# Kernel optimization log

Hardware: AMD Instinct MI355X
Metric: run time of the kernel (lower is better)

## Reference

```python
import jax, jax.numpy as jnp
import numpy as np

B, T, E, H, L = 16, 1024, 1024, 512, 6
C = 1024  # conv out channels


def _lstm_dir(x_tbi, Wih, Whh, bih, bhh):
    # x_tbi: [T, B, I]; single-direction LSTM, PyTorch gate order (i, f, g, o)
    Bn = x_tbi.shape[1]
    Hh = Whh.shape[1]
    b = bih + bhh
    def step(carry, xt):
        h, c = carry
        g = xt @ Wih.T + h @ Whh.T + b  # [B, 4H]
        i, f, gg, o = jnp.split(g, 4, axis=-1)
        c = jax.nn.sigmoid(f) * c + jax.nn.sigmoid(i) * jnp.tanh(gg)
        h = jax.nn.sigmoid(o) * jnp.tanh(c)
        return (h, c), h
    h0 = jnp.zeros((Bn, Hh), x_tbi.dtype)
    _, hs = jax.lax.scan(step, (h0, h0), x_tbi)
    return hs  # [T, B, H]


def _forward(embeddings, attention_mask, labels, conv_w, conv_b, bn_gamma, bn_beta,
             bn_mean, bn_var, lstm_Wih, lstm_Whh, lstm_bih, lstm_bhh,
             cls_w, cls_b, crf_start, crf_end, crf_trans):
    # Conv1d(E->1024, k=5, pad=2) on [B, C, T]
    x = jax.lax.conv_general_dilated(
        embeddings.astype(jnp.float32).transpose(0, 2, 1), conv_w,
        window_strides=(1,), padding=[(2, 2)],
        dimension_numbers=("NCH", "OIH", "NCH")) + conv_b[None, :, None]
    # BatchNorm1d (eval: running stats) fused + ReLU
    scale = bn_gamma / jnp.sqrt(bn_var + 1e-5)
    x = jax.nn.relu(x * scale[None, :, None] + (bn_beta - bn_mean * scale)[None, :, None])
    # time-major for the LSTM scans: [T, B, 1024]
    x = x.transpose(2, 0, 1)
    for l in range(3):
        fw = _lstm_dir(x, lstm_Wih[l, 0], lstm_Whh[l, 0], lstm_bih[l, 0], lstm_bhh[l, 0])
        bw = _lstm_dir(x[::-1], lstm_Wih[l, 1], lstm_Whh[l, 1], lstm_bih[l, 1], lstm_bhh[l, 1])[::-1]
        x = jnp.concatenate([fw, bw], axis=-1)  # [T, B, 2H]
    logits = x @ cls_w.T + cls_b  # [T, B, L]; dropout is identity in eval
    # CRF negative log-likelihood (torchcrf, batch_first handled by time-major layout)
    mask = (attention_mask.astype(bool) & (labels != -100)).T  # [T, B]
    tags = jnp.where(labels == -100, 0, labels).astype(jnp.int32).T  # [T, B]
    mf = mask.astype(logits.dtype)
    bidx = jnp.arange(logits.shape[1])
    # numerator: score of the given tag sequence
    score0 = crf_start[tags[0]] + logits[0, bidx, tags[0]]
    def num_step(carry, inp):
        score, prev = carry
        et, mt, mtf, tt = inp
        s = crf_trans[prev, tt] + et[bidx, tt]
        return (score + mtf * s, jnp.where(mt, tt, prev)), None
    (num, last), _ = jax.lax.scan(
        num_step, (score0, tags[0]), (logits[1:], mask[1:], mf[1:], tags[1:]))
    num = num + crf_end[last]
    # denominator: forward algorithm (log partition)
    def den_step(alpha, inp):
        et, mt = inp
        nxt = jax.nn.logsumexp(alpha[:, :, None] + crf_trans[None, :, :] + et[:, None, :], axis=1)
        return jnp.where(mt[:, None], nxt, alpha), None
    alpha, _ = jax.lax.scan(den_step, crf_start + logits[0], (logits[1:], mask[1:]))
    den = jax.nn.logsumexp(alpha + crf_end, axis=-1)
    return -(num - den).mean()  # reduction='mean' over batch, negated


def setup_inputs() -> dict:
    key = jax.random.key(0)
    ks = jax.random.split(key, 16)
    p = lambda k, shp: jax.random.normal(k, shp, jnp.float32) * 0.05
    return {
        "embeddings": jax.random.normal(ks[0], (B, T, E), jnp.float32),
        "attention_mask": jnp.ones((B, T), jnp.int32),
        "labels": jax.random.randint(ks[1], (B, T), 0, L, jnp.int32),
        "conv_w": p(ks[2], (C, E, 5)),
        "conv_b": p(ks[3], (C,)),
        "bn_gamma": jnp.ones((C,), jnp.float32),
        "bn_beta": jnp.zeros((C,), jnp.float32),
        "bn_mean": p(ks[4], (C,)),
        "bn_var": jax.random.uniform(ks[5], (C,), jnp.float32, 0.5, 1.5),
        "lstm_Wih": p(ks[6], (3, 2, 4 * H, C)),
        "lstm_Whh": p(ks[7], (3, 2, 4 * H, H)),
        "lstm_bih": p(ks[8], (3, 2, 4 * H)),
        "lstm_bhh": p(ks[9], (3, 2, 4 * H)),
        "cls_w": p(ks[10], (L, 2 * H)),
        "cls_b": p(ks[11], (L,)),
        "crf_start": p(ks[12], (L,)),
        "crf_end": p(ks[13], (L,)),
        "crf_trans": p(ks[14], (L, L)),
    }


def reference(embeddings, attention_mask, labels, conv_w, conv_b, bn_gamma, bn_beta,
              bn_mean, bn_var, lstm_Wih, lstm_Whh, lstm_bih, lstm_bhh,
              cls_w, cls_b, crf_start, crf_end, crf_trans):
    return _forward(embeddings, attention_mask, labels, conv_w, conv_b, bn_gamma,
                    bn_beta, bn_mean, bn_var, lstm_Wih, lstm_Whh, lstm_bih,
                    lstm_bhh, cls_w, cls_b, crf_start, crf_end, crf_trans)
```

## Files before the change

kernel.cpp:

```cpp
#include <hip/hip_runtime.h>


typedef short bf16_t;
typedef __attribute__((ext_vector_type(8))) short bf16x8;
typedef __attribute__((ext_vector_type(4))) float f32x4;

__device__ __forceinline__ bf16_t f2b(float x) {
  unsigned u = __float_as_uint(x);
  unsigned r = (u + 0x7fffu + ((u >> 16) & 1u)) >> 16;
  return (bf16_t)(unsigned short)r;
}
__device__ __forceinline__ float blo(unsigned u) { return __uint_as_float(u << 16); }
__device__ __forceinline__ float bhi(unsigned u) { return __uint_as_float(u & 0xffff0000u); }


__global__ void embed_pad_k(const float* __restrict__ E, bf16_t* __restrict__ P) {
  size_t i4 = ((size_t)blockIdx.x * 256 + threadIdx.x) * 4;
  if (i4 >= 16ul * 1028 * 1024) return;
  int e = (int)(i4 & 1023);
  size_t rest = i4 >> 10;
  int tp = (int)(rest % 1028);
  int b  = (int)(rest / 1028);
  bf16_t o[4];
  if (tp >= 2 && tp < 1026) {
    const float4 v = *(const float4*)(E + (((size_t)b * 1024 + (tp - 2)) * 1024 + e));
    o[0] = f2b(v.x); o[1] = f2b(v.y); o[2] = f2b(v.z); o[3] = f2b(v.w);
  } else {
    o[0] = o[1] = o[2] = o[3] = 0;
  }
  *(uint2*)(P + i4) = *(const uint2*)o;
}

__global__ void convw_cvt_k(const float* __restrict__ S, bf16_t* __restrict__ D) {
  int idx = blockIdx.x * 256 + threadIdx.x;
  if (idx >= 1024 * 1024) return;
  int c = idx >> 10, e = idx & 1023;
  const float* s = S + (size_t)idx * 5;
#pragma unroll
  for (int kk = 0; kk < 5; kk++) D[(size_t)c * 5120 + kk * 1024 + e] = f2b(s[kk]);
}

__global__ void bnfold_k(const float* cb, const float* g, const float* be,
                         const float* mn, const float* vr, float* a, float* dd) {
  int c = blockIdx.x * 256 + threadIdx.x;
  if (c < 1024) {
    float s = g[c] * rsqrtf(vr[c] + 1e-5f);
    a[c] = s;
    dd[c] = (cb[c] - mn[c]) * s + be[c];
  }
}

__global__ void wihcvt_k(const float* __restrict__ S, bf16_t* __restrict__ D) {
  size_t i = ((size_t)blockIdx.x * 256 + threadIdx.x) * 4;
  if (i >= 3ul * 2 * 2048 * 1024) return;
  float4 v = *(const float4*)(S + i);
  bf16_t o[4] = {f2b(v.x), f2b(v.y), f2b(v.z), f2b(v.w)};
  *(uint2*)(D + i) = *(const uint2*)o;
}

__global__ __launch_bounds__(256, 1) void gemm_bt(
    const bf16_t* __restrict__ A, const bf16_t* __restrict__ W,
    const float* __restrict__ bias0, const float* __restrict__ bias1,
    bf16_t* __restrict__ C, int M, int N, int K) {
  const int tid = threadIdx.x;
  const int nb = N >> 7;
  const int m0 = (blockIdx.x / nb) * 128, n0 = (blockIdx.x % nb) * 128;
  __shared__ bf16_t As[128][72];
  __shared__ bf16_t Bs[128][72];
  const int wv = tid >> 6, ln = tid & 63;
  const int wm = (wv >> 1) * 64, wn = (wv & 1) * 64;
  const int lb = ln & 15, lq = ln >> 4;
  f32x4 acc[4][4] = {};
  for (int k0 = 0; k0 < K; k0 += 64) {
    __syncthreads();
#pragma unroll
    for (int i = 0; i < 4; i++) {
      int idx = tid + i * 256, r = idx >> 3, ch = idx & 7;
      *(uint4*)&As[r][ch * 8] = *(const uint4*)(A + (size_t)(m0 + r) * K + k0 + ch * 8);
      *(uint4*)&Bs[r][ch * 8] = *(const uint4*)(W + (size_t)(n0 + r) * K + k0 + ch * 8);
    }
    __syncthreads();
#pragma unroll
    for (int kk = 0; kk < 2; kk++) {
      bf16x8 af[4], bfr[4];
#pragma unroll
      for (int t = 0; t < 4; t++) {
        af[t]  = *(const bf16x8*)&As[wm + t * 16 + lb][kk * 32 + lq * 8];
        bfr[t] = *(const bf16x8*)&Bs[wn + t * 16 + lb][kk * 32 + lq * 8];
      }
#pragma unroll
      for (int mt = 0; mt < 4; mt++)
#pragma unroll
        for (int nt = 0; nt < 4; nt++)
          acc[mt][nt] = __builtin_amdgcn_mfma_f32_16x16x32_bf16(af[mt], bfr[nt], acc[mt][nt], 0, 0, 0);
    }
  }
#pragma unroll
  for (int mt = 0; mt < 4; mt++)
#pragma unroll
    for (int nt = 0; nt < 4; nt++) {
      int col = n0 + wn + nt * 16 + lb;
      float bs = bias0[col] + bias1[col];
#pragma unroll
      for (int r = 0; r < 4; r++) {
        int row = m0 + wm + mt * 16 + lq * 4 + r;
        C[(size_t)row * N + col] = f2b(acc[mt][nt][r] + bs);
      }
    }
}

__global__ __launch_bounds__(256, 1) void conv_gemm(
    const bf16_t* __restrict__ EP, const bf16_t* __restrict__ Wc,
    const float* __restrict__ bn_a, const float* __restrict__ bn_d,
    bf16_t* __restrict__ X) {
  const int tid = threadIdx.x;
  const int m0 = (blockIdx.x >> 3) * 128, n0 = (blockIdx.x & 7) * 128;
  __shared__ bf16_t As[128][72];
  __shared__ bf16_t Bs[128][72];
  const int wv = tid >> 6, ln = tid & 63;
  const int wm = (wv >> 1) * 64, wn = (wv & 1) * 64;
  const int lb = ln & 15, lq = ln >> 4;
  f32x4 acc[4][4] = {};
  for (int kk = 0; kk < 5; kk++) {
    for (int k0 = 0; k0 < 1024; k0 += 64) {
      __syncthreads();
#pragma unroll
      for (int i = 0; i < 4; i++) {
        int idx = tid + i * 256, r = idx >> 3, ch = idx & 7;
        int m = m0 + r;
        const bf16_t* ap = EP + ((size_t)((m & 15) * 1028 + (m >> 4) + kk)) * 1024 + k0 + ch * 8;
        *(uint4*)&As[r][ch * 8] = *(const uint4*)ap;
        *(uint4*)&Bs[r][ch * 8] = *(const uint4*)(Wc + (size_t)(n0 + r) * 5120 + kk * 1024 + k0 + ch * 8);
      }
      __syncthreads();
#pragma unroll
      for (int kq = 0; kq < 2; kq++) {
        bf16x8 af[4], bfr[4];
#pragma unroll
        for (int t = 0; t < 4; t++) {
          af[t]  = *(const bf16x8*)&As[wm + t * 16 + lb][kq * 32 + lq * 8];
          bfr[t] = *(const bf16x8*)&Bs[wn + t * 16 + lb][kq * 32 + lq * 8];
        }
#pragma unroll
        for (int mt = 0; mt < 4; mt++)
#pragma unroll
          for (int nt = 0; nt < 4; nt++)
            acc[mt][nt] = __builtin_amdgcn_mfma_f32_16x16x32_bf16(af[mt], bfr[nt], acc[mt][nt], 0, 0, 0);
      }
    }
  }
#pragma unroll
  for (int mt = 0; mt < 4; mt++)
#pragma unroll
    for (int nt = 0; nt < 4; nt++) {
      int col = n0 + wn + nt * 16 + lb;
      float sa = bn_a[col], sd = bn_d[col];
#pragma unroll
      for (int r = 0; r < 4; r++) {
        int row = m0 + wm + mt * 16 + lq * 4 + r;
        float v = fmaxf(acc[mt][nt][r] * sa + sd, 0.f);
        X[(size_t)row * 1024 + col] = f2b(v);
      }
    }
}

__global__ __launch_bounds__(256, 1) void rec_kernel(
    const float* __restrict__ Whh,
    const bf16_t* __restrict__ gfw,
    const bf16_t* __restrict__ gbw,
    bf16_t* __restrict__ xout,
    unsigned long long* __restrict__ hstT,
    float* __restrict__ cst,
    int t0f, int t0b, int nsteps, int tag_base) {
  const int tid = threadIdx.x;
  const int d  = blockIdx.x >> 5;
  const int j0 = (blockIdx.x & 31) << 4;
  const int wv = tid >> 6;
  const int ln = tid & 63;
  const int lb = ln & 15;
  const int lq = ln >> 4;

  __shared__ bf16_t Hb[16][520];
  __shared__ float  Ex[4][16][17];

  bf16x8 afrag[16];
  {
    const float* wrow = Whh + ((size_t)(d * 2048 + wv * 512 + j0 + lb)) * 512;
#pragma unroll
    for (int kk = 0; kk < 16; kk++) {
      const float* wp = wrow + kk * 32 + lq * 8;
      float4 va = *(const float4*)wp;
      float4 vb = *(const float4*)(wp + 4);
      bf16x8 fr;
      fr[0] = f2b(va.x); fr[1] = f2b(va.y); fr[2] = f2b(va.z); fr[3] = f2b(va.w);
      fr[4] = f2b(vb.x); fr[5] = f2b(vb.y); fr[6] = f2b(vb.z); fr[7] = f2b(vb.w);
      afrag[kk] = fr;
    }
  }
  const int cb = tid >> 4;
  const int cj = tid & 15;
  float creg = cst[((size_t)d * 16 + cb) * 512 + j0 + cj];
  const bf16_t* gates = (d == 0) ? gfw : gbw;

  unsigned g0, g1;
  {
    const int trow = (d == 0) ? 0 : (nsteps - 1);
    const unsigned* gp = (const unsigned*)(gates + ((size_t)trow * 16 + lb) * 2048 + wv * 512 + j0 + lq * 4);
    g0 = gp[0]; g1 = gp[1];
  }

  for (int s = 0; s < nsteps; s++) {
    const int rb = (s & 1) ^ 1, wb = s & 1;
    {
      const unsigned long long* src =
          hstT + (((size_t)rb * 2 + d) * 16 + (wv << 2)) * 256;
      const unsigned expect = (unsigned)(tag_base + s);
      unsigned long long v[16];
      bool ok;
      do {
        ok = true;
#pragma unroll
        for (int i = 0; i < 16; i++)
          v[i] = __hip_atomic_load(src + i * 64 + ln, __ATOMIC_RELAXED, __HIP_MEMORY_SCOPE_AGENT);
#pragma unroll
        for (int i = 0; i < 16; i++) ok = ok && ((unsigned)(v[i] >> 32) == expect);
      } while (!__all(ok));
#pragma unroll
      for (int i = 0; i < 16; i++) {
        int idx = i * 64 + ln;
        *(unsigned*)&Hb[(wv << 2) + (idx >> 8)][(idx & 255) * 2] = (unsigned)v[i];
      }
    }
    __syncthreads();
    const int t = (d == 0) ? (t0f + s) : (t0b + nsteps - 1 - s);
    f32x4 acc0, acc1;
    acc0[0] = blo(g0); acc0[1] = bhi(g0); acc0[2] = blo(g1); acc0[3] = bhi(g1);
    acc1[0] = 0.f; acc1[1] = 0.f; acc1[2] = 0.f; acc1[3] = 0.f;
#pragma unroll
    for (int kk = 0; kk < 8; kk++) {
      bf16x8 b0 = *(const bf16x8*)&Hb[lb][(2 * kk) * 32 + lq * 8];
      bf16x8 b1 = *(const bf16x8*)&Hb[lb][(2 * kk + 1) * 32 + lq * 8];
      acc0 = __builtin_amdgcn_mfma_f32_16x16x32_bf16(afrag[2 * kk], b0, acc0, 0, 0, 0);
      acc1 = __builtin_amdgcn_mfma_f32_16x16x32_bf16(afrag[2 * kk + 1], b1, acc1, 0, 0, 0);
    }
    if (s + 1 < nsteps) {
      const int trn = (d == 0) ? (s + 1) : (nsteps - 2 - s);
      const unsigned* gpn = (const unsigned*)(gates + ((size_t)trn * 16 + lb) * 2048 + wv * 512 + j0 + lq * 4);
      g0 = gpn[0]; g1 = gpn[1];
    }
#pragma unroll
    for (int r = 0; r < 4; r++) Ex[wv][lq * 4 + r][lb] = acc0[r] + acc1[r];
    __syncthreads();
    float gi = Ex[0][cj][cb], gf = Ex[1][cj][cb], gg = Ex[2][cj][cb], go = Ex[3][cj][cb];
    float si = 1.f / (1.f + expf(-gi));
    float sf = 1.f / (1.f + expf(-gf));
    float so = 1.f / (1.f + expf(-go));
    creg = sf * creg + si * tanhf(gg);
    float h = so * tanhf(creg);
    bf16_t hb = f2b(h);
    {
      int hi = __shfl_down((int)(unsigned)(unsigned short)hb, 1, 64);
      if ((cj & 1) == 0) {
        unsigned data = (unsigned)(unsigned short)hb | ((unsigned)hi << 16);
        unsigned long long val =
            ((unsigned long long)(unsigned)(tag_base + s + 1) << 32) | data;
        unsigned long long* hp =
            hstT + (((size_t)wb * 2 + d) * 16 + cb) * 256 + ((j0 + cj) >> 1);
        __hip_atomic_store(hp, val, __ATOMIC_RELAXED, __HIP_MEMORY_SCOPE_AGENT);
      }
    }
    xout[((size_t)t * 16 + cb) * 1024 + d * 512 + j0 + cj] = hb;
  }
  cst[((size_t)d * 16 + cb) * 512 + j0 + cj] = creg;
}

__global__ void cls_kernel(const bf16_t* __restrict__ X, const float* __restrict__ Wc,
                           const float* __restrict__ bc, float* __restrict__ Lg) {
  int wv = threadIdx.x >> 6, ln = threadIdx.x & 63;
  size_t m = (size_t)blockIdx.x * 4 + wv;
  const bf16_t* xr = X + m * 1024 + ln * 16;
  uint4 v0 = *(const uint4*)xr;
  uint4 v1 = *(const uint4*)(xr + 8);
  float xv[16];
  const unsigned* p0 = (const unsigned*)&v0;
  const unsigned* p1 = (const unsigned*)&v1;
#pragma unroll
  for (int i = 0; i < 4; i++) { xv[2 * i] = blo(p0[i]); xv[2 * i + 1] = bhi(p0[i]); }
#pragma unroll
  for (int i = 0; i < 4; i++) { xv[8 + 2 * i] = blo(p1[i]); xv[8 + 2 * i + 1] = bhi(p1[i]); }
#pragma unroll
  for (int l = 0; l < 6; l++) {
    const float* wr = Wc + l * 1024 + ln * 16;
    float p = 0.f;
#pragma unroll
    for (int i = 0; i < 16; i++) p += xv[i] * wr[i];
#pragma unroll
    for (int off = 32; off; off >>= 1) p += __shfl_xor(p, off, 64);
    if (ln == 0) Lg[m * 6 + l] = p + bc[l];
  }
}

__global__ void crf_kernel(const float* __restrict__ Lg, const int* __restrict__ attn,
                           const int* __restrict__ labels, const float* __restrict__ start,
                           const float* __restrict__ endw, const float* __restrict__ trans,
                           float* __restrict__ out) {
  int b = blockIdx.x, ln = threadIdx.x;
  __shared__ float str[36];
  __shared__ int tg[1024];
  __shared__ unsigned char mk[1024];
  if (ln < 36) str[ln] = trans[ln];
  for (int t = ln; t < 1024; t += 64) {
    int lab = labels[b * 1024 + t];
    mk[t] = (unsigned char)((attn[b * 1024 + t] != 0) && (lab != -100));
    tg[t] = (lab == -100) ? 0 : lab;
  }
  __syncthreads();
  int j = ln;
  bool act = j < 6;
  float alpha = act ? (start[j] + Lg[(size_t)b * 6 + j]) : -1e30f;
  for (int t = 1; t < 1024; t++) {
    float vv[6], mx = -1e30f;
#pragma unroll
    for (int i = 0; i < 6; i++) {
      float ai = __shfl(alpha, i, 64);
      float v = ai + str[i * 6 + (act ? j : 0)];
      vv[i] = v;
      mx = fmaxf(mx, v);
    }
    float sm = 0.f;
#pragma unroll
    for (int i = 0; i < 6; i++) sm += expf(vv[i] - mx);
    float na = mx + logf(sm) + (act ? Lg[((size_t)t * 16 + b) * 6 + j] : 0.f);
    if (mk[t] && act) alpha = na;
  }
  float z = act ? (alpha + endw[j]) : -1e30f;
  float zm = z;
#pragma unroll
  for (int i = 0; i < 6; i++) zm = fmaxf(zm, __shfl(z, i, 64));
  float zs = act ? expf(z - zm) : 0.f;
  float tot = 0.f;
#pragma unroll
  for (int i = 0; i < 6; i++) tot += __shfl(zs, i, 64);
  float den = zm + logf(tot);
  if (ln == 0) {
    float score = start[tg[0]] + Lg[(size_t)b * 6 + tg[0]];
    int prev = tg[0];
    for (int t = 1; t < 1024; t++) {
      if (mk[t]) {
        score += str[prev * 6 + tg[t]] + Lg[((size_t)t * 16 + b) * 6 + tg[t]];
        prev = tg[t];
      }
    }
    score += endw[prev];
    atomicAdd(out, (den - score) * (1.0f / 16.0f));
  }
}

extern "C" void kernel_launch(void* const* d_in, const int* in_sizes, int n_in,
                              void* d_out, int out_size, void* d_ws, size_t ws_size,
                              hipStream_t stream) {
  const float* emb    = (const float*)d_in[0];
  const int*   attn   = (const int*)d_in[1];
  const int*   labels = (const int*)d_in[2];
  const float* convw  = (const float*)d_in[3];
  const float* convb  = (const float*)d_in[4];
  const float* bng    = (const float*)d_in[5];
  const float* bnb    = (const float*)d_in[6];
  const float* bnm    = (const float*)d_in[7];
  const float* bnv    = (const float*)d_in[8];
  const float* wih    = (const float*)d_in[9];
  const float* whh    = (const float*)d_in[10];
  const float* bih    = (const float*)d_in[11];
  const float* bhh    = (const float*)d_in[12];
  const float* clsw   = (const float*)d_in[13];
  const float* clsb   = (const float*)d_in[14];
  const float* crfs   = (const float*)d_in[15];
  const float* crfe   = (const float*)d_in[16];
  const float* crft   = (const float*)d_in[17];
  (void)in_sizes; (void)n_in; (void)out_size; (void)ws_size;

  char* w = (char*)d_ws;
  auto alloc = [&](size_t bytes) { char* p = w; w += (bytes + 255) & ~(size_t)255; return p; };
  bf16_t* emb_pad = (bf16_t*)alloc(16ul * 1028 * 1024 * 2);
  bf16_t* wconv   = (bf16_t*)alloc(1024ul * 5120 * 2);
  float*  bn_a    = (float*)alloc(4096);
  float*  bn_d    = (float*)alloc(4096);
  bf16_t* wihb    = (bf16_t*)alloc(3ul * 2 * 2048 * 1024 * 2);
  bf16_t* xA      = (bf16_t*)alloc(16384ul * 1024 * 2);
  bf16_t* xB      = (bf16_t*)alloc(16384ul * 1024 * 2);
  bf16_t* gfw     = (bf16_t*)alloc(8192ul * 2048 * 2);
  bf16_t* gbw     = (bf16_t*)alloc(8192ul * 2048 * 2);
  unsigned long long* hstT = (unsigned long long*)alloc(2ul * 2 * 16 * 256 * 8);
  float*  cst     = (float*)alloc(2ul * 16 * 512 * 4);
  float*  lgt     = (float*)alloc(16384ul * 6 * 4);

  hipMemsetAsync(d_out, 0, 4, stream);

  embed_pad_k<<<16448, 256, 0, stream>>>(emb, emb_pad);
  convw_cvt_k<<<4096, 256, 0, stream>>>(convw, wconv);
  bnfold_k<<<4, 256, 0, stream>>>(convb, bng, bnb, bnm, bnv, bn_a, bn_d);
  wihcvt_k<<<12288, 256, 0, stream>>>(wih, wihb);

  conv_gemm<<<128 * 8, 256, 0, stream>>>(emb_pad, wconv, bn_a, bn_d, xA);

  bf16_t* xin = xA;
  bf16_t* xout = xB;
  for (int l = 0; l < 3; l++) {
    hipMemsetAsync(hstT, 0, 2ul * 2 * 16 * 256 * 8, stream);
    hipMemsetAsync(cst, 0, 2ul * 16 * 512 * 4, stream);
    for (int c = 0; c < 2; c++) {
      int t0f = c * 512, t0b = (1 - c) * 512;
      gemm_bt<<<64 * 16, 256, 0, stream>>>(
          xin + (size_t)t0f * 16 * 1024, wihb + ((size_t)l * 2 + 0) * 2048 * 1024,
          bih + (l * 2 + 0) * 2048, bhh + (l * 2 + 0) * 2048, gfw, 8192, 2048, 1024);
      gemm_bt<<<64 * 16, 256, 0, stream>>>(
          xin + (size_t)t0b * 16 * 1024, wihb + ((size_t)l * 2 + 1) * 2048 * 1024,
          bih + (l * 2 + 1) * 2048, bhh + (l * 2 + 1) * 2048, gbw, 8192, 2048, 1024);
      rec_kernel<<<64, 256, 0, stream>>>(whh + (size_t)l * 2 * 2048 * 512,
                                         gfw, gbw, xout, hstT, cst, t0f, t0b, 512, c * 512);
    }
    bf16_t* tmp = xin; xin = xout; xout = tmp;
  }

  cls_kernel<<<4096, 256, 0, stream>>>(xin, clsw, clsb, lgt);
  crf_kernel<<<16, 64, 0, stream>>>(lgt, attn, labels, crfs, crfe, crft, (float*)d_out);
}
```

Baseline: 9.208 ms.

## Interleave LSTM gate rows so each lane holds i,f,g,o and drop LDS exchange

The W_hh rows loaded into each wave's MFMA fragments are permuted so that the four gate outputs of one hidden unit land in the same lane's accumulator. This removes the per-step LDS exchange buffer and the second __syncthreads in the recurrent loop. The input-gate GEMM epilogue now writes gates in a [t][j][b][gate] layout so each lane fetches its four gate preactivations with one 8-byte load. The spin-wait also re-polls only the entries whose tags are stale. The cost is scattered 2-byte stores in the GEMM epilogue and a changed hidden-state packing via a shuffle across lanes 16 apart.

After: 11.84 ms. 1.29x slower.

```diff
diff --git a/kernel.cpp b/kernel.cpp
--- a/kernel.cpp
+++ b/kernel.cpp
@@ -58,26 +58,25 @@
   *(uint2*)(D + i) = *(const uint2*)o;
 }
 
-__global__ __launch_bounds__(256, 1) void gemm_bt(
+__global__ __launch_bounds__(256, 1) void gemm_gates(
     const bf16_t* __restrict__ A, const bf16_t* __restrict__ W,
     const float* __restrict__ bias0, const float* __restrict__ bias1,
-    bf16_t* __restrict__ C, int M, int N, int K) {
+    bf16_t* __restrict__ G) {
   const int tid = threadIdx.x;
-  const int nb = N >> 7;
-  const int m0 = (blockIdx.x / nb) * 128, n0 = (blockIdx.x % nb) * 128;
+  const int m0 = (blockIdx.x >> 4) * 128, n0 = (blockIdx.x & 15) * 128;
   __shared__ bf16_t As[128][72];
   __shared__ bf16_t Bs[128][72];
   const int wv = tid >> 6, ln = tid & 63;
   const int wm = (wv >> 1) * 64, wn = (wv & 1) * 64;
   const int lb = ln & 15, lq = ln >> 4;
   f32x4 acc[4][4] = {};
-  for (int k0 = 0; k0 < K; k0 += 64) {
+  for (int k0 = 0; k0 < 1024; k0 += 64) {
     __syncthreads();
 #pragma unroll
     for (int i = 0; i < 4; i++) {
       int idx = tid + i * 256, r = idx >> 3, ch = idx & 7;
-      *(uint4*)&As[r][ch * 8] = *(const uint4*)(A + (size_t)(m0 + r) * K + k0 + ch * 8);
-      *(uint4*)&Bs[r][ch * 8] = *(const uint4*)(W + (size_t)(n0 + r) * K + k0 + ch * 8);
+      *(uint4*)&As[r][ch * 8] = *(const uint4*)(A + (size_t)(m0 + r) * 1024 + k0 + ch * 8);
+      *(uint4*)&Bs[r][ch * 8] = *(const uint4*)(W + (size_t)(n0 + r) * 1024 + k0 + ch * 8);
     }
     __syncthreads();
 #pragma unroll
@@ -100,11 +99,13 @@
 #pragma unroll
     for (int nt = 0; nt < 4; nt++) {
       int col = n0 + wn + nt * 16 + lb;
+      int g = col >> 9, j = col & 511;
       float bs = bias0[col] + bias1[col];
 #pragma unroll
       for (int r = 0; r < 4; r++) {
         int row = m0 + wm + mt * 16 + lq * 4 + r;
-        C[(size_t)row * N + col] = f2b(acc[mt][nt][r] + bs);
+        int t = row >> 4, b = row & 15;
+        G[(((size_t)t * 512 + j) * 16 + b) * 4 + g] = f2b(acc[mt][nt][r] + bs);
       }
     }
 }
@@ -166,8 +167,8 @@
 
 __global__ __launch_bounds__(256, 1) void rec_kernel(
     const float* __restrict__ Whh,
-    const bf16_t* __restrict__ gfw,
-    const bf16_t* __restrict__ gbw,
+    const bf16_t* __restrict__ Gfw,
+    const bf16_t* __restrict__ Gbw,
     bf16_t* __restrict__ xout,
     unsigned long long* __restrict__ hstT,
     float* __restrict__ cst,
@@ -180,12 +181,12 @@
   const int lb = ln & 15;
   const int lq = ln >> 4;
 
-  __shared__ bf16_t Hb[16][520];
-  __shared__ float  Ex[4][16][17];
+  __shared__ bf16_t Hb[16][514];
 
   bf16x8 afrag[16];
   {
-    const float* wrow = Whh + ((size_t)(d * 2048 + wv * 512 + j0 + lb)) * 512;
+    const float* wrow =
+        Whh + ((size_t)(d * 2048 + (lb & 3) * 512 + j0 + wv * 4 + (lb >> 2))) * 512;
 #pragma unroll
     for (int kk = 0; kk < 16; kk++) {
       const float* wp = wrow + kk * 32 + lq * 8;
@@ -197,16 +198,14 @@
       afrag[kk] = fr;
     }
   }
-  const int cb = tid >> 4;
-  const int cj = tid & 15;
-  float creg = cst[((size_t)d * 16 + cb) * 512 + j0 + cj];
-  const bf16_t* gates = (d == 0) ? gfw : gbw;
-
-  unsigned g0, g1;
+  const int jme = j0 + wv * 4 + lq;
+  float creg = cst[((size_t)d * 16 + lb) * 512 + jme];
+  const bf16_t* G = (d == 0) ? Gfw : Gbw;
+
+  uint2 gv;
   {
     const int trow = (d == 0) ? 0 : (nsteps - 1);
-    const unsigned* gp = (const unsigned*)(gates + ((size_t)trow * 16 + lb) * 2048 + wv * 512 + j0 + lq * 4);
-    g0 = gp[0]; g1 = gp[1];
+    gv = *(const uint2*)(G + (((size_t)trow * 512 + jme) * 16 + lb) * 4);
   }
 
   for (int s = 0; s < nsteps; s++) {
@@ -216,15 +215,19 @@
           hstT + (((size_t)rb * 2 + d) * 16 + (wv << 2)) * 256;
       const unsigned expect = (unsigned)(tag_base + s);
       unsigned long long v[16];
-      bool ok;
-      do {
-        ok = true;
+#pragma unroll
+      for (int i = 0; i < 16; i++)
+        v[i] = __hip_atomic_load(src + i * 64 + ln, __ATOMIC_RELAXED, __HIP_MEMORY_SCOPE_AGENT);
+      while (true) {
+        bool ok = true;
+#pragma unroll
+        for (int i = 0; i < 16; i++) ok = ok && ((unsigned)(v[i] >> 32) == expect);
+        if (__all(ok)) break;
 #pragma unroll
         for (int i = 0; i < 16; i++)
-          v[i] = __hip_atomic_load(src + i * 64 + ln, __ATOMIC_RELAXED, __HIP_MEMORY_SCOPE_AGENT);
-#pragma unroll
-        for (int i = 0; i < 16; i++) ok = ok && ((unsigned)(v[i] >> 32) == expect);
-      } while (!__all(ok));
+          if ((unsigned)(v[i] >> 32) != expect)
+            v[i] = __hip_atomic_load(src + i * 64 + ln, __ATOMIC_RELAXED, __HIP_MEMORY_SCOPE_AGENT);
+      }
 #pragma unroll
       for (int i = 0; i < 16; i++) {
         int idx = i * 64 + ln;
@@ -234,7 +237,7 @@
     __syncthreads();
     const int t = (d == 0) ? (t0f + s) : (t0b + nsteps - 1 - s);
     f32x4 acc0, acc1;
-    acc0[0] = blo(g0); acc0[1] = bhi(g0); acc0[2] = blo(g1); acc0[3] = bhi(g1);
+    acc0[0] = blo(gv.x); acc0[1] = bhi(gv.x); acc0[2] = blo(gv.y); acc0[3] = bhi(gv.y);
     acc1[0] = 0.f; acc1[1] = 0.f; acc1[2] = 0.f; acc1[3] = 0.f;
 #pragma unroll
     for (int kk = 0; kk < 8; kk++) {
@@ -245,13 +248,10 @@
     }
     if (s + 1 < nsteps) {
       const int trn = (d == 0) ? (s + 1) : (nsteps - 2 - s);
-      const unsigned* gpn = (const unsigned*)(gates + ((size_t)trn * 16 + lb) * 2048 + wv * 512 + j0 + lq * 4);
-      g0 = gpn[0]; g1 = gpn[1];
-    }
-#pragma unroll
-    for (int r = 0; r < 4; r++) Ex[wv][lq * 4 + r][lb] = acc0[r] + acc1[r];
-    __syncthreads();
-    float gi = Ex[0][cj][cb], gf = Ex[1][cj][cb], gg = Ex[2][cj][cb], go = Ex[3][cj][cb];
+      gv = *(const uint2*)(G + (((size_t)trn * 512 + jme) * 16 + lb) * 4);
+    }
+    float gi = acc0[0] + acc1[0], gf = acc0[1] + acc1[1];
+    float gg = acc0[2] + acc1[2], go = acc0[3] + acc1[3];
     float si = 1.f / (1.f + expf(-gi));
     float sf = 1.f / (1.f + expf(-gf));
     float so = 1.f / (1.f + expf(-go));
@@ -259,19 +259,20 @@
     float h = so * tanhf(creg);
     bf16_t hb = f2b(h);
     {
-      int hi = __shfl_down((int)(unsigned)(unsigned short)hb, 1, 64);
-      if ((cj & 1) == 0) {
-        unsigned data = (unsigned)(unsigned short)hb | ((unsigned)hi << 16);
+      unsigned hu = (unsigned)(unsigned short)hb;
+      unsigned hp = (unsigned)__shfl_down((int)hu, 16, 64);
+      if ((lq & 1) == 0) {
+        unsigned data = hu | (hp << 16);
         unsigned long long val =
             ((unsigned long long)(unsigned)(tag_base + s + 1) << 32) | data;
-        unsigned long long* hp =
-            hstT + (((size_t)wb * 2 + d) * 16 + cb) * 256 + ((j0 + cj) >> 1);
-        __hip_atomic_store(hp, val, __ATOMIC_RELAXED, __HIP_MEMORY_SCOPE_AGENT);
-      }
-    }
-    xout[((size_t)t * 16 + cb) * 1024 + d * 512 + j0 + cj] = hb;
-  }
-  cst[((size_t)d * 16 + cb) * 512 + j0 + cj] = creg;
+        unsigned long long* dst =
+            hstT + (((size_t)wb * 2 + d) * 16 + lb) * 256 + (jme >> 1);
+        __hip_atomic_store(dst, val, __ATOMIC_RELAXED, __HIP_MEMORY_SCOPE_AGENT);
+      }
+    }
+    xout[((size_t)t * 16 + lb) * 1024 + d * 512 + jme] = hb;
+  }
+  cst[((size_t)d * 16 + lb) * 512 + jme] = creg;
 }
 
 __global__ void cls_kernel(const bf16_t* __restrict__ X, const float* __restrict__ Wc,
@@ -388,8 +389,8 @@
   bf16_t* wihb    = (bf16_t*)alloc(3ul * 2 * 2048 * 1024 * 2);
   bf16_t* xA      = (bf16_t*)alloc(16384ul * 1024 * 2);
   bf16_t* xB      = (bf16_t*)alloc(16384ul * 1024 * 2);
-  bf16_t* gfw     = (bf16_t*)alloc(8192ul * 2048 * 2);
-  bf16_t* gbw     = (bf16_t*)alloc(8192ul * 2048 * 2);
+  bf16_t* gfw     = (bf16_t*)alloc(512ul * 512 * 16 * 4 * 2);
+  bf16_t* gbw     = (bf16_t*)alloc(512ul * 512 * 16 * 4 * 2);
   unsigned long long* hstT = (unsigned long long*)alloc(2ul * 2 * 16 * 256 * 8);
   float*  cst     = (float*)alloc(2ul * 16 * 512 * 4);
   float*  lgt     = (float*)alloc(16384ul * 6 * 4);
@@ -410,12 +411,12 @@
     hipMemsetAsync(cst, 0, 2ul * 16 * 512 * 4, stream);
     for (int c = 0; c < 2; c++) {
       int t0f = c * 512, t0b = (1 - c) * 512;
-      gemm_bt<<<64 * 16, 256, 0, stream>>>(
+      gemm_gates<<<64 * 16, 256, 0, stream>>>(
           xin + (size_t)t0f * 16 * 1024, wihb + ((size_t)l * 2 + 0) * 2048 * 1024,
-          bih + (l * 2 + 0) * 2048, bhh + (l * 2 + 0) * 2048, gfw, 8192, 2048, 1024);
-      gemm_bt<<<64 * 16, 256, 0, stream>>>(
+          bih + (l * 2 + 0) * 2048, bhh + (l * 2 + 0) * 2048, gfw);
+      gemm_gates<<<64 * 16, 256, 0, stream>>>(
           xin + (size_t)t0b * 16 * 1024, wihb + ((size_t)l * 2 + 1) * 2048 * 1024,
-          bih + (l * 2 + 1) * 2048, bhh + (l * 2 + 1) * 2048, gbw, 8192, 2048, 1024);
+          bih + (l * 2 + 1) * 2048, bhh + (l * 2 + 1) * 2048, gbw);
       rec_kernel<<<64, 256, 0, stream>>>(whh + (size_t)l * 2 * 2048 * 512,
                                          gfw, gbw, xout, hstT, cst, t0f, t0b, 512, c * 512);
     }
```
